# Kernel optimization log

Hardware: AMD Instinct MI355X
Metric: run time of the kernel (lower is better)

## Reference

```python
import jax, jax.numpy as jnp
import numpy as np

B, C, D, H = 1024, 119, 1024, 16
DH = D // H  # head dim = 64
EPS = 1e-5


def setup_inputs() -> dict:
    key = jax.random.key(0)
    ks = jax.random.split(key, 16)
    s = lambda n: 1.0 / np.sqrt(n)
    return {
        "board_tensor": jax.random.normal(ks[0], (B, C, 8, 8), jnp.float32),
        "emb_W": jax.random.normal(ks[1], (C, D), jnp.float32) * s(C),
        "emb_b": jnp.zeros((D,), jnp.float32),
        "positional": jnp.zeros((1, 64, D), jnp.float32),
        "Wq": jax.random.normal(ks[2], (D, D), jnp.float32) * s(D),
        "bq": jnp.zeros((D,), jnp.float32),
        "Wk": jax.random.normal(ks[3], (D, D), jnp.float32) * s(D),
        "bk": jnp.zeros((D,), jnp.float32),
        "Wv": jax.random.normal(ks[4], (D, D), jnp.float32) * s(D),
        "bv": jnp.zeros((D,), jnp.float32),
        "Wo": jax.random.normal(ks[5], (D, D), jnp.float32) * s(D),
        "bo": jnp.zeros((D,), jnp.float32),
        "rel_bias": jax.random.normal(ks[6], (H, 64, 64), jnp.float32) * 0.02,
        "ln_g": jnp.ones((D,), jnp.float32),
        "ln_b": jnp.zeros((D,), jnp.float32),
    }


def _layernorm(x, g, b):
    mu = jnp.mean(x, axis=-1, keepdims=True)
    var = jnp.mean(jnp.square(x - mu), axis=-1, keepdims=True)
    return (x - mu) * jax.lax.rsqrt(var + EPS) * g + b


def reference(board_tensor, emb_W, emb_b, positional, Wq, bq, Wk, bk, Wv, bv,
              Wo, bo, rel_bias, ln_g, ln_b):
    b = board_tensor.shape[0]
    # (B, C, 8, 8) -> (B, 64, C)
    x = board_tensor.reshape(b, C, 64).transpose(0, 2, 1)
    x = x @ emb_W + emb_b            # embedding GEMM -> (B, 64, D)
    x = x + positional
    # chess relative attention with learned per-head 64x64 bias
    q = (x @ Wq + bq).reshape(b, 64, H, DH)
    k = (x @ Wk + bk).reshape(b, 64, H, DH)
    v = (x @ Wv + bv).reshape(b, 64, H, DH)
    scores = jnp.einsum('bqhd,bkhd->bhqk', q, k) / np.sqrt(DH) + rel_bias
    attn = jax.nn.softmax(scores, axis=-1)
    o = jnp.einsum('bhqk,bkhd->bqhd', attn, v).reshape(b, 64, D)
    o = o @ Wo + bo
    # residual + LayerNorm
    return _layernorm(x + o, ln_g, ln_b)
```

## Files before the change

kernel.cpp:

```cpp
#include <hip/hip_runtime.h>
#include <hip/hip_bf16.h>
#include <stdint.h>


typedef float  floatx4 __attribute__((ext_vector_type(4)));
typedef short  bf16x8  __attribute__((ext_vector_type(8)));
typedef short  bf16x4  __attribute__((ext_vector_type(4)));

__device__ __forceinline__ short f2bf(float f) {
  __hip_bfloat16 h = __float2bfloat16(f);
  return *reinterpret_cast<short*>(&h);
}
__device__ __forceinline__ float bf2f(short s) {
  union { float f; uint32_t u; } c;
  c.u = ((uint32_t)(uint16_t)s) << 16;
  return c.f;
}
__device__ __forceinline__ floatx4 mfma16(bf16x8 a, bf16x8 b, floatx4 c) {
  return __builtin_amdgcn_mfma_f32_16x16x32_bf16(a, b, c, 0, 0, 0);
}

#define ASYNC_CP16(gsrc, ldst)                                                 \
  __builtin_amdgcn_global_load_lds(                                            \
      (const __attribute__((address_space(1))) void*)(gsrc),                   \
      (__attribute__((address_space(3))) void*)(ldst), 16, 0, 0)

__global__ void k_transpose_bf16(const float* __restrict__ src,
                                 short* __restrict__ dst) {
  __shared__ float tile[32][33];
  const int bx = blockIdx.x * 32, by = blockIdx.y * 32;
  const int tx = threadIdx.x, ty = threadIdx.y;
#pragma unroll
  for (int i = 0; i < 32; i += 8)
    tile[ty + i][tx] = src[(size_t)(by + ty + i) * 1024 + bx + tx];
  __syncthreads();
#pragma unroll
  for (int i = 0; i < 32; i += 8)
    dst[(size_t)(bx + ty + i) * 1024 + by + tx] = f2bf(tile[tx][ty + i]);
}

__global__ void k_embWt(const float* __restrict__ embW, short* __restrict__ dst) {
  const int idx = blockIdx.x * 256 + threadIdx.x;
  const int n = idx >> 7, c = idx & 127;
  dst[idx] = f2bf((c < 119) ? embW[(size_t)c * 1024 + n] : 0.f);
}

__global__ __launch_bounds__(256) void k_embed(
    const float* __restrict__ board, const short* __restrict__ embWt,
    const float* __restrict__ emb_b, const float* __restrict__ pos,
    short* __restrict__ x) {
  __shared__ short As[64 * 136];
  __shared__ short Bs[128 * 32];
  const int t = threadIdx.x, l = t & 63, w = t >> 6;
  const int quad = l >> 4, lan = l & 15;
  const int xcd = blockIdx.x & 7;
  const int lin = (blockIdx.x >> 3) + xcd * 1024;
  const int b = lin >> 3, nBase = (lin & 7) << 7;
  const float* bb = board + (size_t)b * (119 * 64);
  const int s = t & 63;
#pragma unroll
  for (int it = 0; it < 16; ++it) {
    const int c0 = ((t >> 6) + it * 4) * 2;
    float u0 = (c0 < 119) ? bb[c0 * 64 + s] : 0.f;
    float u1 = (c0 + 1 < 119) ? bb[(c0 + 1) * 64 + s] : 0.f;
    short2 pr; pr.x = f2bf(u0); pr.y = f2bf(u1);
    *(short2*)&As[s * 136 + c0] = pr;
  }
  const short* Bg0 = embWt + (size_t)(nBase + (t >> 2)) * 128 + (t & 3) * 8;
  const short* Bg1 = Bg0 + (size_t)64 * 128;
  short* Bs0 = &Bs[(w * 16) * 32];
  short* Bs1 = &Bs[(64 + w * 16) * 32];
  floatx4 acc[4][2] = {};
  __syncthreads();
  for (int kk = 0; kk < 4; ++kk) {
    ASYNC_CP16(Bg0 + kk * 32, Bs0);
    ASYNC_CP16(Bg1 + kk * 32, Bs1);
    __syncthreads();
    bf16x8 af[4], bfr[2];
#pragma unroll
    for (int mt = 0; mt < 4; ++mt)
      af[mt] = *(const bf16x8*)&As[(mt * 16 + lan) * 136 + kk * 32 + quad * 8];
#pragma unroll
    for (int n2 = 0; n2 < 2; ++n2)
      bfr[n2] = *(const bf16x8*)&Bs[(w * 32 + n2 * 16 + lan) * 32 + quad * 8];
#pragma unroll
    for (int mt = 0; mt < 4; ++mt)
#pragma unroll
      for (int n2 = 0; n2 < 2; ++n2)
        acc[mt][n2] = mfma16(af[mt], bfr[n2], acc[mt][n2]);
    __syncthreads();
  }
#pragma unroll
  for (int n2 = 0; n2 < 2; ++n2) {
    const int n = nBase + w * 32 + n2 * 16 + lan;
    const float bi = emb_b[n];
#pragma unroll
    for (int mt = 0; mt < 4; ++mt) {
      const int s0 = mt * 16 + quad * 4;
      floatx4 v = acc[mt][n2];
#pragma unroll
      for (int r = 0; r < 4; ++r) {
        const int ss = s0 + r;
        x[((size_t)b * 64 + ss) * 1024 + n] = f2bf(v[r] + bi + pos[ss * 1024 + n]);
      }
    }
  }
}

__global__ __launch_bounds__(256) void k_gemm_qkv(
    const short* __restrict__ A, const short* __restrict__ Bt,
    const float* __restrict__ bq, const float* __restrict__ bk,
    const float* __restrict__ bv, short* __restrict__ qb,
    short* __restrict__ kb, short* __restrict__ vtb) {
  __shared__ short As[128 * 32];
  __shared__ short Bs[128 * 32];
  const int t = threadIdx.x, l = t & 63, w = t >> 6;
  const int quad = l >> 4, lan = l & 15;
  const int xcd = blockIdx.x & 7;
  const int lin = (blockIdx.x >> 3) + xcd * 1536;
  const int grp = lin / 192;
  const int rem = lin - grp * 192;
  const int mBase = ((grp << 3) + (rem & 7)) << 7;
  const int nBase = (rem >> 3) << 7;
  const int wm = w >> 1, wn = w & 1;

  const short* Ag0 = A + (size_t)(mBase + (t >> 2)) * 1024 + (t & 3) * 8;
  const short* Ag1 = Ag0 + (size_t)64 * 1024;
  const short* Bg0 = Bt + (size_t)(nBase + (t >> 2)) * 1024 + (t & 3) * 8;
  const short* Bg1 = Bg0 + (size_t)64 * 1024;
  short* As0 = &As[(w * 16) * 32];
  short* As1 = &As[(64 + w * 16) * 32];
  short* Bs0 = &Bs[(w * 16) * 32];
  short* Bs1 = &Bs[(64 + w * 16) * 32];

  floatx4 acc[4][4] = {};
  for (int kk = 0; kk < 32; ++kk) {
    const int ko = kk * 32;
    ASYNC_CP16(Ag0 + ko, As0);
    ASYNC_CP16(Ag1 + ko, As1);
    ASYNC_CP16(Bg0 + ko, Bs0);
    ASYNC_CP16(Bg1 + ko, Bs1);
    __syncthreads();
    bf16x8 af[4], bfr[4];
#pragma unroll
    for (int mt = 0; mt < 4; ++mt)
      af[mt] = *(const bf16x8*)&As[(wm * 64 + mt * 16 + lan) * 32 + quad * 8];
#pragma unroll
    for (int nt = 0; nt < 4; ++nt)
      bfr[nt] = *(const bf16x8*)&Bs[(wn * 64 + nt * 16 + lan) * 32 + quad * 8];
#pragma unroll
    for (int mt = 0; mt < 4; ++mt)
#pragma unroll
      for (int nt = 0; nt < 4; ++nt)
        acc[mt][nt] = mfma16(af[mt], bfr[nt], acc[mt][nt]);
    __syncthreads();
  }
  const int region = nBase >> 10;
  const int nb = nBase & 1023;
  const float* bias = (region == 0) ? bq : (region == 1) ? bk : bv;
  short* qk = (region == 0) ? qb : kb;
#pragma unroll
  for (int nt = 0; nt < 4; ++nt) {
    const int nn = nb + wn * 64 + nt * 16 + lan;
    const int h = nn >> 6, dh = nn & 63;
    const float bi = bias[nn];
#pragma unroll
    for (int mt = 0; mt < 4; ++mt) {
      const int m0 = mBase + wm * 64 + mt * 16 + quad * 4;
      const int b = m0 >> 6, s0 = m0 & 63;
      floatx4 v = acc[mt][nt];
      if (region < 2) {
        short* dst = qk + (((size_t)b * 16 + h) * 64 + s0) * 64 + dh;
        dst[0]   = f2bf(v.x + bi);
        dst[64]  = f2bf(v.y + bi);
        dst[128] = f2bf(v.z + bi);
        dst[192] = f2bf(v.w + bi);
      } else {
        bf16x4 pk = {f2bf(v.x + bi), f2bf(v.y + bi), f2bf(v.z + bi), f2bf(v.w + bi)};
        *(bf16x4*)(vtb + (((size_t)b * 16 + h) * 64 + dh) * 64 + s0) = pk;
      }
    }
  }
}

__global__ __launch_bounds__(256) void k_attn(
    const short* __restrict__ qb, const short* __restrict__ kb,
    const short* __restrict__ vtb, const float* __restrict__ rel_bias,
    short* __restrict__ ob) {
  __shared__ short P[4][64 * 72];
  const int t = threadIdx.x, l = t & 63, w = t >> 6;
  const int quad = l >> 4, lan = l & 15;
  const int b = blockIdx.x >> 2;
  const int h = (blockIdx.x & 3) * 4 + w;
  const short* q  = qb  + ((size_t)b * 16 + h) * 4096;
  const short* kp = kb  + ((size_t)b * 16 + h) * 4096;
  const short* vt = vtb + ((size_t)b * 16 + h) * 4096;
  const float* bias = rel_bias + (size_t)h * 4096;
  short* Pw = &P[w][0];

  bf16x8 kf[4][2], qf[4][2];
#pragma unroll
  for (int mt = 0; mt < 4; ++mt) {
    kf[mt][0] = *(const bf16x8*)&kp[(mt * 16 + lan) * 64 + quad * 8];
    kf[mt][1] = *(const bf16x8*)&kp[(mt * 16 + lan) * 64 + 32 + quad * 8];
  }
#pragma unroll
  for (int nt = 0; nt < 4; ++nt) {
    qf[nt][0] = *(const bf16x8*)&q[(nt * 16 + lan) * 64 + quad * 8];
    qf[nt][1] = *(const bf16x8*)&q[(nt * 16 + lan) * 64 + 32 + quad * 8];
  }
  floatx4 S[4][4];
#pragma unroll
  for (int mt = 0; mt < 4; ++mt)
#pragma unroll
    for (int nt = 0; nt < 4; ++nt) {
      floatx4 z = {0.f, 0.f, 0.f, 0.f};
      z = mfma16(kf[mt][0], qf[nt][0], z);
      S[mt][nt] = mfma16(kf[mt][1], qf[nt][1], z);
    }
  float rs[4];
#pragma unroll
  for (int nt = 0; nt < 4; ++nt) {
    const int qi = nt * 16 + lan;
    float sv[4][4];
    float m = -1e30f;
#pragma unroll
    for (int mt = 0; mt < 4; ++mt) {
      floatx4 bi = *(const floatx4*)&bias[qi * 64 + mt * 16 + quad * 4];
#pragma unroll
      for (int r = 0; r < 4; ++r) {
        sv[mt][r] = fmaf(S[mt][nt][r], 0.125f, bi[r]);
        m = fmaxf(m, sv[mt][r]);
      }
    }
    m = fmaxf(m, __shfl_xor(m, 16));
    m = fmaxf(m, __shfl_xor(m, 32));
    float sum = 0.f;
#pragma unroll
    for (int mt = 0; mt < 4; ++mt) {
      float p0 = exp2f((sv[mt][0] - m) * 1.4426950408889634f);
      float p1 = exp2f((sv[mt][1] - m) * 1.4426950408889634f);
      float p2 = exp2f((sv[mt][2] - m) * 1.4426950408889634f);
      float p3 = exp2f((sv[mt][3] - m) * 1.4426950408889634f);
      sum += p0 + p1 + p2 + p3;
      bf16x4 pk = {f2bf(p0), f2bf(p1), f2bf(p2), f2bf(p3)};
      *(bf16x4*)&Pw[qi * 72 + mt * 16 + quad * 4] = pk;
    }
    sum += __shfl_xor(sum, 16);
    sum += __shfl_xor(sum, 32);
    rs[nt] = 1.0f / sum;
  }
  bf16x8 pf[4][2];
#pragma unroll
  for (int nt = 0; nt < 4; ++nt) {
    pf[nt][0] = *(const bf16x8*)&Pw[(nt * 16 + lan) * 72 + quad * 8];
    pf[nt][1] = *(const bf16x8*)&Pw[(nt * 16 + lan) * 72 + 32 + quad * 8];
  }
#pragma unroll
  for (int mo = 0; mo < 4; ++mo) {
    bf16x8 vf0 = *(const bf16x8*)&vt[(mo * 16 + lan) * 64 + quad * 8];
    bf16x8 vf1 = *(const bf16x8*)&vt[(mo * 16 + lan) * 64 + 32 + quad * 8];
#pragma unroll
    for (int nt = 0; nt < 4; ++nt) {
      floatx4 z = {0.f, 0.f, 0.f, 0.f};
      z = mfma16(vf0, pf[nt][0], z);
      z = mfma16(vf1, pf[nt][1], z);
      const int qi = nt * 16 + lan;
      const int dh0 = mo * 16 + quad * 4;
      const float r = rs[nt];
      bf16x4 pk = {f2bf(z.x * r), f2bf(z.y * r), f2bf(z.z * r), f2bf(z.w * r)};
      *(bf16x4*)&ob[((size_t)b * 64 + qi) * 1024 + h * 64 + dh0] = pk;
    }
  }
}

__global__ __launch_bounds__(256) void k_gemm_oproj(
    const short* __restrict__ A, const short* __restrict__ Bt,
    const float* __restrict__ bo, const short* __restrict__ xres,
    short* __restrict__ y) {
  __shared__ short As[128 * 32];
  __shared__ short Bs[128 * 32];
  const int t = threadIdx.x, l = t & 63, w = t >> 6;
  const int quad = l >> 4, lan = l & 15;
  const int xcd = blockIdx.x & 7;
  const int lin = (blockIdx.x >> 3) + xcd * 512;
  const int grp = lin >> 6;
  const int rem = lin & 63;
  const int mBase = ((grp << 3) + (rem & 7)) << 7;
  const int nBase = (rem >> 3) << 7;
  const int wm = w >> 1, wn = w & 1;

  const short* Ag0 = A + (size_t)(mBase + (t >> 2)) * 1024 + (t & 3) * 8;
  const short* Ag1 = Ag0 + (size_t)64 * 1024;
  const short* Bg0 = Bt + (size_t)(nBase + (t >> 2)) * 1024 + (t & 3) * 8;
  const short* Bg1 = Bg0 + (size_t)64 * 1024;
  short* As0 = &As[(w * 16) * 32];
  short* As1 = &As[(64 + w * 16) * 32];
  short* Bs0 = &Bs[(w * 16) * 32];
  short* Bs1 = &Bs[(64 + w * 16) * 32];

  floatx4 acc[4][4] = {};
  for (int kk = 0; kk < 32; ++kk) {
    const int ko = kk * 32;
    ASYNC_CP16(Ag0 + ko, As0);
    ASYNC_CP16(Ag1 + ko, As1);
    ASYNC_CP16(Bg0 + ko, Bs0);
    ASYNC_CP16(Bg1 + ko, Bs1);
    __syncthreads();
    bf16x8 af[4], bfr[4];
#pragma unroll
    for (int mt = 0; mt < 4; ++mt)
      af[mt] = *(const bf16x8*)&As[(wm * 64 + mt * 16 + lan) * 32 + quad * 8];
#pragma unroll
    for (int nt = 0; nt < 4; ++nt)
      bfr[nt] = *(const bf16x8*)&Bs[(wn * 64 + nt * 16 + lan) * 32 + quad * 8];
#pragma unroll
    for (int mt = 0; mt < 4; ++mt)
#pragma unroll
      for (int nt = 0; nt < 4; ++nt)
        acc[mt][nt] = mfma16(af[mt], bfr[nt], acc[mt][nt]);
    __syncthreads();
  }
#pragma unroll
  for (int nt = 0; nt < 4; ++nt) {
    const int n = nBase + wn * 64 + nt * 16 + lan;
    const float bi = bo[n];
#pragma unroll
    for (int mt = 0; mt < 4; ++mt) {
      const int m0 = mBase + wm * 64 + mt * 16 + quad * 4;
      floatx4 v = acc[mt][nt];
#pragma unroll
      for (int r = 0; r < 4; ++r) {
        const size_t idx = (size_t)(m0 + r) * 1024 + n;
        y[idx] = f2bf(v[r] + bi + bf2f(xres[idx]));
      }
    }
  }
}

__global__ __launch_bounds__(256) void k_ln(
    const short* __restrict__ y, const float* __restrict__ g,
    const float* __restrict__ be, float* __restrict__ out) {
  const int row = blockIdx.x;
  const int t = threadIdx.x;
  const short* yr = y + (size_t)row * 1024;
  bf16x4 v4 = *(const bf16x4*)&yr[t * 4];
  float v0 = bf2f(v4.x), v1 = bf2f(v4.y), v2 = bf2f(v4.z), v3 = bf2f(v4.w);
  float s = v0 + v1 + v2 + v3;
  float s2 = v0 * v0 + v1 * v1 + v2 * v2 + v3 * v3;
#pragma unroll
  for (int off = 1; off < 64; off <<= 1) {
    s  += __shfl_xor(s, off);
    s2 += __shfl_xor(s2, off);
  }
  __shared__ float red[8];
  const int w = t >> 6;
  if ((t & 63) == 0) { red[w] = s; red[w + 4] = s2; }
  __syncthreads();
  s  = red[0] + red[1] + red[2] + red[3];
  s2 = red[4] + red[5] + red[6] + red[7];
  const float mu = s * (1.f / 1024.f);
  const float var = s2 * (1.f / 1024.f) - mu * mu;
  const float rstd = rsqrtf(var + 1e-5f);
  const int c = t * 4;
  float4 o;
  o.x = (v0 - mu) * rstd * g[c]     + be[c];
  o.y = (v1 - mu) * rstd * g[c + 1] + be[c + 1];
  o.z = (v2 - mu) * rstd * g[c + 2] + be[c + 2];
  o.w = (v3 - mu) * rstd * g[c + 3] + be[c + 3];
  *(float4*)&out[(size_t)row * 1024 + c] = o;
}

extern "C" void kernel_launch(void* const* d_in, const int* in_sizes, int n_in,
                              void* d_out, int out_size, void* d_ws,
                              size_t ws_size, hipStream_t stream) {
  const float* board    = (const float*)d_in[0];
  const float* emb_W    = (const float*)d_in[1];
  const float* emb_b    = (const float*)d_in[2];
  const float* pos      = (const float*)d_in[3];
  const float* Wq       = (const float*)d_in[4];
  const float* bq       = (const float*)d_in[5];
  const float* Wk       = (const float*)d_in[6];
  const float* bk       = (const float*)d_in[7];
  const float* Wv       = (const float*)d_in[8];
  const float* bv       = (const float*)d_in[9];
  const float* Wo       = (const float*)d_in[10];
  const float* bo       = (const float*)d_in[11];
  const float* rel_bias = (const float*)d_in[12];
  const float* ln_g     = (const float*)d_in[13];
  const float* ln_b     = (const float*)d_in[14];

  char* ws = (char*)d_ws;
  short* Wqkv_t = (short*)ws; ws += (size_t)3072 * 1024 * 2;
  short* Wo_t   = (short*)ws; ws += (size_t)1024 * 1024 * 2;
  short* embWt  = (short*)ws; ws += (size_t)1024 * 128 * 2;
  short* xb     = (short*)ws; ws += (size_t)65536 * 1024 * 2;
  short* qb     = (short*)ws; ws += (size_t)16384 * 4096 * 2;
  short* kb     = (short*)ws; ws += (size_t)16384 * 4096 * 2;
  short* vtb    = (short*)ws; ws += (size_t)16384 * 4096 * 2;
  short* ob     = (short*)ws; ws += (size_t)65536 * 1024 * 2;
  short* yb     = kb;

  dim3 tb(32, 8);
  k_transpose_bf16<<<dim3(32, 32), tb, 0, stream>>>(Wq, Wqkv_t);
  k_transpose_bf16<<<dim3(32, 32), tb, 0, stream>>>(Wk, Wqkv_t + (size_t)1024 * 1024);
  k_transpose_bf16<<<dim3(32, 32), tb, 0, stream>>>(Wv, Wqkv_t + (size_t)2 * 1024 * 1024);
  k_transpose_bf16<<<dim3(32, 32), tb, 0, stream>>>(Wo, Wo_t);
  k_embWt<<<512, 256, 0, stream>>>(emb_W, embWt);

  k_embed<<<8192, 256, 0, stream>>>(board, embWt, emb_b, pos, xb);
  k_gemm_qkv<<<12288, 256, 0, stream>>>(xb, Wqkv_t, bq, bk, bv, qb, kb, vtb);
  k_attn<<<4096, 256, 0, stream>>>(qb, kb, vtb, rel_bias, ob);
  k_gemm_oproj<<<4096, 256, 0, stream>>>(ob, Wo_t, bo, xb, yb);
  k_ln<<<65536, 256, 0, stream>>>(yb, ln_g, ln_b, (float*)d_out);
}
```

Measured before the change: 1.350 ms.

## Replace QKV and output-projection GEMMs with 256x256 pipelined 8-wave kernel

Both projection GEMMs now use a shared core with 256x256 block tiles, 512 threads, a BK=64 tile staged in two halves into double-buffered LDS, and an XOR swizzle against bank conflicts. Async global-to-LDS copies for the next tiles are interleaved with MFMA phases using sched barriers, s_setprio, and explicit vmcnt waits. The aim is more reuse per loaded byte and overlap of loads with matrix math, removing the serialized load/sync/compute loop of the 128x128 kernels. The cost is 128KB of LDS per block and heavy register use (32 accumulators per lane), with occupancy limited to the launch bound of two blocks.

Measured after the change: 1.359 ms. No clear change (+0.7%).

```diff
diff --git a/kernel.cpp b/kernel.cpp
--- a/kernel.cpp
+++ b/kernel.cpp
@@ -107,68 +107,135 @@
   }
 }
 
-__global__ __launch_bounds__(256) void k_gemm_qkv(
+__device__ __forceinline__ void gemm8_core(
+    const short* __restrict__ A, const short* __restrict__ Bt,
+    short* lds, const int mBase, const int nBase, floatx4 (&acc)[8][4]) {
+  const int t = threadIdx.x;
+  const int w = t >> 6, l = t & 63;
+  const int lan = l & 15, quad = l >> 4;
+  const int wm = w >> 2, wn = w & 3;
+  const int row0 = t >> 2;
+  const int sg = (t & 3) ^ ((t >> 3) & 3);
+  const short* Ag = A + (size_t)(mBase + row0) * 1024 + sg * 8;
+  const short* Bg = Bt + (size_t)(nBase + row0) * 1024 + sg * 8;
+  const int swz = (quad ^ ((lan >> 1) & 3)) * 8;
+  const int aRd = (wm * 128 + lan) * 32 + swz;
+  const int bRd = 32768 + (wn * 64 + lan) * 32 + swz;
+  const int wst = w * 512;
+
+#define STAGE_A8(ktgt, kh, buf) do {                                          \
+    const short* _s = Ag + (ktgt) * 64 + (kh) * 32;                           \
+    ASYNC_CP16(_s,          &lds[(buf) * 16384 + (kh) * 8192 + wst]);          \
+    ASYNC_CP16(_s + 131072, &lds[(buf) * 16384 + (kh) * 8192 + 4096 + wst]);   \
+  } while (0)
+#define STAGE_B8(ktgt, kh, buf) do {                                          \
+    const short* _s = Bg + (ktgt) * 64 + (kh) * 32;                           \
+    ASYNC_CP16(_s,          &lds[32768 + (buf) * 16384 + (kh) * 8192 + wst]);  \
+    ASYNC_CP16(_s + 131072,                                                    \
+               &lds[32768 + (buf) * 16384 + (kh) * 8192 + 4096 + wst]);        \
+  } while (0)
+#define LDA8(dst, buf, ks, mh)                                                \
+    _Pragma("unroll") for (int mf = 0; mf < 4; ++mf)                          \
+      dst[mf] = *(const bf16x8*)&lds[(buf) * 16384 + (ks) * 8192 + aRd +      \
+                                     ((mh) * 64 + mf * 16) * 32];
+#define LDB8(dst, buf, ks)                                                    \
+    _Pragma("unroll") for (int nf = 0; nf < 4; ++nf)                          \
+      dst[nf] = *(const bf16x8*)&lds[(buf) * 16384 + (ks) * 8192 + bRd +      \
+                                     nf * 512];
+#define MMA8(mh, bfr)                                                         \
+    _Pragma("unroll") for (int mf = 0; mf < 4; ++mf)                          \
+      _Pragma("unroll") for (int nf = 0; nf < 4; ++nf)                        \
+        acc[(mh) * 4 + mf][nf] = mfma16(af[mf], bfr[nf], acc[(mh) * 4 + mf][nf]);
+#define PHASE_MID                                                             \
+    __builtin_amdgcn_sched_barrier(0);                                        \
+    __builtin_amdgcn_s_barrier();                                             \
+    asm volatile("s_waitcnt lgkmcnt(0)" ::: "memory");                        \
+    __builtin_amdgcn_sched_barrier(0);                                        \
+    __builtin_amdgcn_s_setprio(1)
+#define PHASE_END                                                             \
+    __builtin_amdgcn_s_setprio(0);                                            \
+    __builtin_amdgcn_sched_barrier(0);                                        \
+    __builtin_amdgcn_s_barrier()
+
+  STAGE_A8(0, 0, 0); STAGE_B8(0, 0, 0);
+  STAGE_A8(0, 1, 0); STAGE_B8(0, 1, 0);
+  STAGE_A8(1, 0, 1); STAGE_B8(1, 0, 1);
+  asm volatile("s_waitcnt vmcnt(4)" ::: "memory");
+  __builtin_amdgcn_sched_barrier(0);
+  __builtin_amdgcn_s_barrier();
+
+#define TILE8(kt, cur) do {                                                   \
+    const int k1 = ((kt) + 1 < 16) ? (kt) + 1 : 15;                           \
+    const int k2 = ((kt) + 2 < 16) ? (kt) + 2 : 15;                           \
+    bf16x8 af[4], bf0[4], bf1[4];                                             \
+                                                          \
+    LDA8(af, cur, 0, 0); LDB8(bf0, cur, 0);                                   \
+    STAGE_A8(k1, 1, (cur) ^ 1);                                               \
+    PHASE_MID; MMA8(0, bf0); PHASE_END;                                       \
+                                                          \
+    LDA8(af, cur, 0, 1);                                                      \
+    STAGE_B8(k1, 1, (cur) ^ 1);                                               \
+    PHASE_MID; MMA8(1, bf0); PHASE_END;                                       \
+                                                          \
+    LDA8(af, cur, 1, 0); LDB8(bf1, cur, 1);                                   \
+    STAGE_A8(k2, 0, cur);                                                     \
+    PHASE_MID; MMA8(0, bf1); PHASE_END;                                       \
+                                                          \
+    LDA8(af, cur, 1, 1);                                                      \
+    STAGE_B8(k2, 0, cur);                                                     \
+    asm volatile("s_waitcnt vmcnt(4)" ::: "memory");                          \
+    PHASE_MID; MMA8(1, bf1); PHASE_END;                                       \
+  } while (0)
+
+#pragma unroll 1
+  for (int it = 0; it < 8; ++it) {
+    TILE8(it * 2, 0);
+    TILE8(it * 2 + 1, 1);
+  }
+  asm volatile("s_waitcnt vmcnt(0)" ::: "memory");
+#undef TILE8
+#undef PHASE_END
+#undef PHASE_MID
+#undef MMA8
+#undef LDB8
+#undef LDA8
+#undef STAGE_B8
+#undef STAGE_A8
+}
+
+__global__ __launch_bounds__(512, 2) void k_gemm_qkv8(
     const short* __restrict__ A, const short* __restrict__ Bt,
     const float* __restrict__ bq, const float* __restrict__ bk,
     const float* __restrict__ bv, short* __restrict__ qb,
     short* __restrict__ kb, short* __restrict__ vtb) {
-  __shared__ short As[128 * 32];
-  __shared__ short Bs[128 * 32];
-  const int t = threadIdx.x, l = t & 63, w = t >> 6;
-  const int quad = l >> 4, lan = l & 15;
+  __shared__ short lds[65536];
   const int xcd = blockIdx.x & 7;
-  const int lin = (blockIdx.x >> 3) + xcd * 1536;
-  const int grp = lin / 192;
-  const int rem = lin - grp * 192;
-  const int mBase = ((grp << 3) + (rem & 7)) << 7;
-  const int nBase = (rem >> 3) << 7;
-  const int wm = w >> 1, wn = w & 1;
-
-  const short* Ag0 = A + (size_t)(mBase + (t >> 2)) * 1024 + (t & 3) * 8;
-  const short* Ag1 = Ag0 + (size_t)64 * 1024;
-  const short* Bg0 = Bt + (size_t)(nBase + (t >> 2)) * 1024 + (t & 3) * 8;
-  const short* Bg1 = Bg0 + (size_t)64 * 1024;
-  short* As0 = &As[(w * 16) * 32];
-  short* As1 = &As[(64 + w * 16) * 32];
-  short* Bs0 = &Bs[(w * 16) * 32];
-  short* Bs1 = &Bs[(64 + w * 16) * 32];
-
-  floatx4 acc[4][4] = {};
-  for (int kk = 0; kk < 32; ++kk) {
-    const int ko = kk * 32;
-    ASYNC_CP16(Ag0 + ko, As0);
-    ASYNC_CP16(Ag1 + ko, As1);
-    ASYNC_CP16(Bg0 + ko, Bs0);
-    ASYNC_CP16(Bg1 + ko, Bs1);
-    __syncthreads();
-    bf16x8 af[4], bfr[4];
-#pragma unroll
-    for (int mt = 0; mt < 4; ++mt)
-      af[mt] = *(const bf16x8*)&As[(wm * 64 + mt * 16 + lan) * 32 + quad * 8];
-#pragma unroll
-    for (int nt = 0; nt < 4; ++nt)
-      bfr[nt] = *(const bf16x8*)&Bs[(wn * 64 + nt * 16 + lan) * 32 + quad * 8];
-#pragma unroll
-    for (int mt = 0; mt < 4; ++mt)
-#pragma unroll
-      for (int nt = 0; nt < 4; ++nt)
-        acc[mt][nt] = mfma16(af[mt], bfr[nt], acc[mt][nt]);
-    __syncthreads();
-  }
+  const int lin = (blockIdx.x >> 3) + xcd * 384;
+  const int grp = lin / 96;
+  const int rem = lin - grp * 96;
+  const int mBase = ((grp << 3) + (rem & 7)) << 8;
+  const int nBase = (rem >> 3) << 8;
+
+  floatx4 acc[8][4] = {};
+  gemm8_core(A, Bt, lds, mBase, nBase, acc);
+
+  const int t = threadIdx.x, w = t >> 6, l = t & 63;
+  const int lan = l & 15, quad = l >> 4;
+  const int wm = w >> 2, wn = w & 3;
   const int region = nBase >> 10;
   const int nb = nBase & 1023;
   const float* bias = (region == 0) ? bq : (region == 1) ? bk : bv;
   short* qk = (region == 0) ? qb : kb;
 #pragma unroll
-  for (int nt = 0; nt < 4; ++nt) {
-    const int nn = nb + wn * 64 + nt * 16 + lan;
-    const int h = nn >> 6, dh = nn & 63;
-    const float bi = bias[nn];
-#pragma unroll
-    for (int mt = 0; mt < 4; ++mt) {
-      const int m0 = mBase + wm * 64 + mt * 16 + quad * 4;
-      const int b = m0 >> 6, s0 = m0 & 63;
-      floatx4 v = acc[mt][nt];
+  for (int am = 0; am < 8; ++am) {
+    const int m0 = mBase + wm * 128 + am * 16 + quad * 4;
+    const int b = m0 >> 6, s0 = m0 & 63;
+#pragma unroll
+    for (int nf = 0; nf < 4; ++nf) {
+      const int nn = nb + wn * 64 + nf * 16 + lan;
+      const int h = nn >> 6, dh = nn & 63;
+      const float bi = bias[nn];
+      floatx4 v = acc[am][nf];
       if (region < 2) {
         short* dst = qk + (((size_t)b * 16 + h) * 64 + s0) * 64 + dh;
         dst[0]   = f2bf(v.x + bi);
@@ -178,6 +245,41 @@
       } else {
         bf16x4 pk = {f2bf(v.x + bi), f2bf(v.y + bi), f2bf(v.z + bi), f2bf(v.w + bi)};
         *(bf16x4*)(vtb + (((size_t)b * 16 + h) * 64 + dh) * 64 + s0) = pk;
+      }
+    }
+  }
+}
+
+__global__ __launch_bounds__(512, 2) void k_gemm_oproj8(
+    const short* __restrict__ A, const short* __restrict__ Bt,
+    const float* __restrict__ bo, const short* __restrict__ xres,
+    short* __restrict__ y) {
+  __shared__ short lds[65536];
+  const int xcd = blockIdx.x & 7;
+  const int lin = (blockIdx.x >> 3) + xcd * 128;
+  const int grp = lin >> 5;
+  const int rem = lin & 31;
+  const int mBase = ((grp << 3) + (rem & 7)) << 8;
+  const int nBase = (rem >> 3) << 8;
+
+  floatx4 acc[8][4] = {};
+  gemm8_core(A, Bt, lds, mBase, nBase, acc);
+
+  const int t = threadIdx.x, w = t >> 6, l = t & 63;
+  const int lan = l & 15, quad = l >> 4;
+  const int wm = w >> 2, wn = w & 3;
+#pragma unroll
+  for (int nf = 0; nf < 4; ++nf) {
+    const int n = nBase + wn * 64 + nf * 16 + lan;
+    const float bi = bo[n];
+#pragma unroll
+    for (int am = 0; am < 8; ++am) {
+      const int m0 = mBase + wm * 128 + am * 16 + quad * 4;
+      floatx4 v = acc[am][nf];
+#pragma unroll
+      for (int r = 0; r < 4; ++r) {
+        const size_t idx = (size_t)(m0 + r) * 1024 + n;
+        y[idx] = f2bf(v[r] + bi + bf2f(xres[idx]));
       }
     }
   }
@@ -270,70 +372,6 @@
       const float r = rs[nt];
       bf16x4 pk = {f2bf(z.x * r), f2bf(z.y * r), f2bf(z.z * r), f2bf(z.w * r)};
       *(bf16x4*)&ob[((size_t)b * 64 + qi) * 1024 + h * 64 + dh0] = pk;
-    }
-  }
-}
-
-__global__ __launch_bounds__(256) void k_gemm_oproj(
-    const short* __restrict__ A, const short* __restrict__ Bt,
-    const float* __restrict__ bo, const short* __restrict__ xres,
-    short* __restrict__ y) {
-  __shared__ short As[128 * 32];
-  __shared__ short Bs[128 * 32];
-  const int t = threadIdx.x, l = t & 63, w = t >> 6;
-  const int quad = l >> 4, lan = l & 15;
-  const int xcd = blockIdx.x & 7;
-  const int lin = (blockIdx.x >> 3) + xcd * 512;
-  const int grp = lin >> 6;
-  const int rem = lin & 63;
-  const int mBase = ((grp << 3) + (rem & 7)) << 7;
-  const int nBase = (rem >> 3) << 7;
-  const int wm = w >> 1, wn = w & 1;
-
-  const short* Ag0 = A + (size_t)(mBase + (t >> 2)) * 1024 + (t & 3) * 8;
-  const short* Ag1 = Ag0 + (size_t)64 * 1024;
-  const short* Bg0 = Bt + (size_t)(nBase + (t >> 2)) * 1024 + (t & 3) * 8;
-  const short* Bg1 = Bg0 + (size_t)64 * 1024;
-  short* As0 = &As[(w * 16) * 32];
-  short* As1 = &As[(64 + w * 16) * 32];
-  short* Bs0 = &Bs[(w * 16) * 32];
-  short* Bs1 = &Bs[(64 + w * 16) * 32];
-
-  floatx4 acc[4][4] = {};
-  for (int kk = 0; kk < 32; ++kk) {
-    const int ko = kk * 32;
-    ASYNC_CP16(Ag0 + ko, As0);
-    ASYNC_CP16(Ag1 + ko, As1);
-    ASYNC_CP16(Bg0 + ko, Bs0);
-    ASYNC_CP16(Bg1 + ko, Bs1);
-    __syncthreads();
-    bf16x8 af[4], bfr[4];
-#pragma unroll
-    for (int mt = 0; mt < 4; ++mt)
-      af[mt] = *(const bf16x8*)&As[(wm * 64 + mt * 16 + lan) * 32 + quad * 8];
-#pragma unroll
-    for (int nt = 0; nt < 4; ++nt)
-      bfr[nt] = *(const bf16x8*)&Bs[(wn * 64 + nt * 16 + lan) * 32 + quad * 8];
-#pragma unroll
-    for (int mt = 0; mt < 4; ++mt)
-#pragma unroll
-      for (int nt = 0; nt < 4; ++nt)
-        acc[mt][nt] = mfma16(af[mt], bfr[nt], acc[mt][nt]);
-    __syncthreads();
-  }
-#pragma unroll
-  for (int nt = 0; nt < 4; ++nt) {
-    const int n = nBase + wn * 64 + nt * 16 + lan;
-    const float bi = bo[n];
-#pragma unroll
-    for (int mt = 0; mt < 4; ++mt) {
-      const int m0 = mBase + wm * 64 + mt * 16 + quad * 4;
-      floatx4 v = acc[mt][nt];
-#pragma unroll
-      for (int r = 0; r < 4; ++r) {
-        const size_t idx = (size_t)(m0 + r) * 1024 + n;
-        y[idx] = f2bf(v[r] + bi + bf2f(xres[idx]));
-      }
     }
   }
 }
@@ -409,8 +447,8 @@
   k_embWt<<<512, 256, 0, stream>>>(emb_W, embWt);
 
   k_embed<<<8192, 256, 0, stream>>>(board, embWt, emb_b, pos, xb);
-  k_gemm_qkv<<<12288, 256, 0, stream>>>(xb, Wqkv_t, bq, bk, bv, qb, kb, vtb);
+  k_gemm_qkv8<<<3072, 512, 0, stream>>>(xb, Wqkv_t, bq, bk, bv, qb, kb, vtb);
   k_attn<<<4096, 256, 0, stream>>>(qb, kb, vtb, rel_bias, ob);
-  k_gemm_oproj<<<4096, 256, 0, stream>>>(ob, Wo_t, bo, xb, yb);
+  k_gemm_oproj8<<<1024, 512, 0, stream>>>(ob, Wo_t, bo, xb, yb);
   k_ln<<<65536, 256, 0, stream>>>(yb, ln_g, ln_b, (float*)d_out);
 }
```
